# Performance work log

Measured on AMD Instinct MI355X. Metric: run time of the kernel, lower is better.

## Reference

```python
import jax, jax.numpy as jnp
import numpy as np

N_HEADS = 16

def setup_inputs() -> dict:
    key = jax.random.key(0)
    ks = jax.random.split(key, 4)
    B, T, C = 4, 2048, 1024
    x = jax.random.normal(ks[0], (B, T, C), dtype=jnp.float32)
    w_qkv = jax.random.normal(ks[1], (C, 3 * C), dtype=jnp.float32) * (1.0 / np.sqrt(C))
    b_qkv = jnp.zeros((3 * C,), dtype=jnp.float32)
    w_proj = jax.random.normal(ks[2], (C, C), dtype=jnp.float32) * (1.0 / np.sqrt(C))
    b_proj = jnp.zeros((C,), dtype=jnp.float32)
    return {"x": x, "w_qkv": w_qkv, "b_qkv": b_qkv, "w_proj": w_proj, "b_proj": b_proj}

def reference(x, w_qkv, b_qkv, w_proj, b_proj):
    B, T, C = x.shape
    H = N_HEADS
    d = C // H
    qkv = x @ w_qkv + b_qkv                       # [B,T,3C]
    q, k, v = jnp.split(qkv, 3, axis=-1)
    # [B,T,C] -> [B,H,T,d]
    q = q.reshape(B, T, H, d).transpose(0, 2, 1, 3)
    k = k.reshape(B, T, H, d).transpose(0, 2, 1, 3)
    v = v.reshape(B, T, H, d).transpose(0, 2, 1, 3)
    scale = 1.0 / np.sqrt(d).astype(np.float32)
    logits = jnp.einsum('bhqd,bhkd->bhqk', q, k) * scale  # [B,H,T,T]
    causal = jnp.tril(jnp.ones((T, T), dtype=bool))
    logits = jnp.where(causal, logits, jnp.finfo(logits.dtype).min)
    attn = jax.nn.softmax(logits, axis=-1)
    out = jnp.einsum('bhqk,bhkd->bhqd', attn, v)          # [B,H,T,d]
    out = out.transpose(0, 2, 1, 3).reshape(B, T, C)
    return out @ w_proj + b_proj
```

## Files before the change

### kernel.cpp

```cpp
#include <hip/hip_runtime.h>
#include <hip/hip_bf16.h>


typedef unsigned short u16;
typedef __bf16 bf16_t;
typedef bf16_t bf16x8 __attribute__((ext_vector_type(8)));
typedef float f32x4 __attribute__((ext_vector_type(4)));
typedef u16 u16x8 __attribute__((ext_vector_type(8)));
typedef const __attribute__((address_space(1))) void* as1cv;
typedef __attribute__((address_space(3))) void* as3v;

#define BB 4
#define TT 2048
#define CC 1024
#define HH 16
#define DD 64

static __device__ __forceinline__ u16 f2bf(float f) {
  union { float f; unsigned int u; } x; x.f = f;
  unsigned int u = x.u;
  u += 0x7fff + ((u >> 16) & 1);
  return (u16)(u >> 16);
}

static __device__ __forceinline__ unsigned int pack2(float lo, float hi) {
  return __builtin_amdgcn_perm(__float_as_uint(hi), __float_as_uint(lo),
                               0x07060302u);
}

__global__ __launch_bounds__(256) void prep(
    const float* __restrict__ x, u16* __restrict__ xb,
    const float* __restrict__ w_qkv, u16* __restrict__ wqkvT,
    const float* __restrict__ w_proj, u16* __restrict__ wprojT) {
  __shared__ float tile[32][33];
  const int id = blockIdx.x;
  if (id < 8192) {
    int i = (id * 256 + threadIdx.x) * 4;
    float4 v = *(const float4*)(x + i);
    ushort4 o;
    o.x = f2bf(v.x); o.y = f2bf(v.y); o.z = f2bf(v.z); o.w = f2bf(v.w);
    *(ushort4*)(xb + i) = o;
    return;
  }
  const float* in; u16* out; int N, n0, k0;
  if (id < 11264) {
    int i = id - 8192;
    in = w_qkv; out = wqkvT; N = 3072;
    n0 = (i % 96) * 32; k0 = (i / 96) * 32;
  } else {
    int i = id - 11264;
    in = w_proj; out = wprojT; N = 1024;
    n0 = (i & 31) * 32; k0 = (i >> 5) * 32;
  }
  const int tx = threadIdx.x & 31, ty = threadIdx.x >> 5;
#pragma unroll
  for (int i = 0; i < 32; i += 8)
    tile[ty + i][tx] = in[(size_t)(k0 + ty + i) * N + n0 + tx];
  __syncthreads();
#pragma unroll
  for (int i = 0; i < 32; i += 8)
    out[(size_t)(n0 + ty + i) * 1024 + k0 + tx] = f2bf(tile[tx][ty + i]);
}

__global__ __launch_bounds__(256) void gemm_bt(
    const u16* __restrict__ A, const u16* __restrict__ Bt,
    const float* __restrict__ bias,
    int M, int N, int K, int mode,
    u16* __restrict__ qb, u16* __restrict__ kb, u16* __restrict__ vt,
    float* __restrict__ outf) {
  __shared__ u16 As[128][64];
  __shared__ u16 Bs[128][64];
  const int tid = threadIdx.x;
  const int lane = tid & 63, wave = tid >> 6;
  const int quad = lane >> 4, l16 = lane & 15;
  const int wy = wave >> 1, wx = wave & 1;
  const int mpc = (M >> 7) >> 3;
  const int id = blockIdx.x;
  const int xcd = id & 7, w = id >> 3;
  const int mi = xcd * mpc + (w % mpc);
  const int ni = w / mpc;
  const int m0 = mi * 128, n0 = ni * 128;
  const int srow = lane >> 3, sblk = (lane & 7) ^ (lane >> 3);
  const int rsw = l16 & 7;

  f32x4 acc[4][4] = {};

  for (int k0 = 0; k0 < K; k0 += 64) {
#pragma unroll
    for (int i = 0; i < 4; i++) {
      int lr = wave * 32 + i * 8;
      int row = lr + srow;
      __builtin_amdgcn_global_load_lds(
          (as1cv)(A + (size_t)(m0 + row) * K + k0 + sblk * 8),
          (as3v)(&As[lr][0]), 16, 0, 0);
      __builtin_amdgcn_global_load_lds(
          (as1cv)(Bt + (size_t)(n0 + row) * K + k0 + sblk * 8),
          (as3v)(&Bs[lr][0]), 16, 0, 0);
    }
    __syncthreads();
#pragma unroll
    for (int ks = 0; ks < 2; ks++) {
      const int pcol = ((ks * 4 + quad) ^ rsw) * 8;
      bf16x8 af[4], bfr[4];
#pragma unroll
      for (int i = 0; i < 4; i++)
        af[i] = *(const bf16x8*)&As[wy * 64 + i * 16 + l16][pcol];
#pragma unroll
      for (int j = 0; j < 4; j++)
        bfr[j] = *(const bf16x8*)&Bs[wx * 64 + j * 16 + l16][pcol];
#pragma unroll
      for (int i = 0; i < 4; i++)
#pragma unroll
        for (int j = 0; j < 4; j++)
          acc[i][j] = __builtin_amdgcn_mfma_f32_16x16x32_bf16(af[i], bfr[j], acc[i][j], 0, 0, 0);
    }
    __syncthreads();
  }

  if (mode == 1) {
#pragma unroll
    for (int i = 0; i < 4; i++)
#pragma unroll
      for (int j = 0; j < 4; j++) {
        int nn = n0 + wx * 64 + j * 16 + l16;
        float bv = bias[nn];
#pragma unroll
        for (int r = 0; r < 4; r++) {
          int mm = m0 + wy * 64 + i * 16 + quad * 4 + r;
          outf[(size_t)mm * N + nn] = acc[i][j][r] + bv;
        }
      }
  } else {
    const int b = m0 >> 11;
    const int tb = (m0 & 2047) + wy * 64 + quad * 4;
    if (n0 < 1024) {
#pragma unroll
      for (int j = 0; j < 4; j++) {
        int nn = n0 + wx * 64 + j * 16 + l16;
        int h = nn >> 6, dd = nn & 63;
        float bv = bias[nn];
        u16* base = qb + ((size_t)(b * HH + h) * TT) * DD + dd;
#pragma unroll
        for (int i = 0; i < 4; i++)
#pragma unroll
          for (int r = 0; r < 4; r++)
            base[(size_t)(tb + i * 16 + r) * DD] =
                f2bf((acc[i][j][r] + bv) * 0.1803368801111f);
      }
    } else if (n0 < 2048) {
#pragma unroll
      for (int j = 0; j < 4; j++) {
        int nn = n0 + wx * 64 + j * 16 + l16;
        int rem = nn & 1023, h = rem >> 6, dd = rem & 63;
        float bv = bias[nn];
        u16* base = kb + ((size_t)(b * HH + h) * TT) * DD + dd;
#pragma unroll
        for (int i = 0; i < 4; i++)
#pragma unroll
          for (int r = 0; r < 4; r++)
            base[(size_t)(tb + i * 16 + r) * DD] = f2bf(acc[i][j][r] + bv);
      }
    } else {
#pragma unroll
      for (int j = 0; j < 4; j++) {
        int nn = n0 + wx * 64 + j * 16 + l16;
        int rem = nn & 1023, h = rem >> 6, dd = rem & 63;
        float bv = bias[nn];
        u16* base = vt + ((size_t)(b * HH + h) * DD + dd) * TT;
#pragma unroll
        for (int i = 0; i < 4; i++)
#pragma unroll
          for (int r = 0; r < 4; r++)
            base[tb + i * 16 + r] = f2bf(acc[i][j][r] + bv);
      }
    }
  }
}

__global__ __launch_bounds__(256) void gemm_proj64(
    const u16* __restrict__ A, const u16* __restrict__ Bt,
    const float* __restrict__ bias, float* __restrict__ outf) {
  constexpr int N = 1024, K = 1024;
  __shared__ u16 As[64][64];
  __shared__ u16 Bs[128][64];
  const int tid = threadIdx.x;
  const int lane = tid & 63, wave = tid >> 6;
  const int quad = lane >> 4, l16 = lane & 15;
  const int wy = wave >> 1, wx = wave & 1;
  const int id = blockIdx.x;
  const int xcd = id & 7, w = id >> 3;
  const int m0 = (xcd * 16 + (w & 15)) * 64, n0 = (w >> 4) * 128;
  const int srow = lane >> 3, sblk = (lane & 7) ^ (lane >> 3);
  const int rsw = l16 & 7;

  f32x4 acc[2][4] = {};

  for (int k0 = 0; k0 < K; k0 += 64) {
#pragma unroll
    for (int i = 0; i < 2; i++) {
      int lr = wave * 16 + i * 8;
      __builtin_amdgcn_global_load_lds(
          (as1cv)(A + (size_t)(m0 + lr + srow) * K + k0 + sblk * 8),
          (as3v)(&As[lr][0]), 16, 0, 0);
    }
#pragma unroll
    for (int i = 0; i < 4; i++) {
      int lr = wave * 32 + i * 8;
      __builtin_amdgcn_global_load_lds(
          (as1cv)(Bt + (size_t)(n0 + lr + srow) * K + k0 + sblk * 8),
          (as3v)(&Bs[lr][0]), 16, 0, 0);
    }
    __syncthreads();
#pragma unroll
    for (int ks = 0; ks < 2; ks++) {
      const int pcol = ((ks * 4 + quad) ^ rsw) * 8;
      bf16x8 af[2], bfr[4];
#pragma unroll
      for (int i = 0; i < 2; i++)
        af[i] = *(const bf16x8*)&As[wy * 32 + i * 16 + l16][pcol];
#pragma unroll
      for (int j = 0; j < 4; j++)
        bfr[j] = *(const bf16x8*)&Bs[wx * 64 + j * 16 + l16][pcol];
#pragma unroll
      for (int i = 0; i < 2; i++)
#pragma unroll
        for (int j = 0; j < 4; j++)
          acc[i][j] = __builtin_amdgcn_mfma_f32_16x16x32_bf16(af[i], bfr[j], acc[i][j], 0, 0, 0);
    }
    __syncthreads();
  }

#pragma unroll
  for (int i = 0; i < 2; i++)
#pragma unroll
    for (int j = 0; j < 4; j++) {
      int nn = n0 + wx * 64 + j * 16 + l16;
      float bv = bias[nn];
#pragma unroll
      for (int r = 0; r < 4; r++) {
        int mm = m0 + wy * 32 + i * 16 + quad * 4 + r;
        outf[(size_t)mm * N + nn] = acc[i][j][r] + bv;
      }
    }
}

__global__ __launch_bounds__(256, 3) void attn_kernel(
    const u16* __restrict__ q_buf, const u16* __restrict__ k_buf,
    const u16* __restrict__ v_t, u16* __restrict__ attn_out) {
  __shared__ __align__(16) u16 Ks[2][64][64];
  __shared__ __align__(16) u16 Vs[2][64][64];
  __shared__ __align__(16) u16 Pl[4][2][16][64];
  const int tid = threadIdx.x;
  const int lane = tid & 63, wave = tid >> 6;
  const int quad = lane >> 4, l16 = lane & 15;
  const int bh = blockIdx.x;
  const int b = bh >> 4, h = bh & 15;
  const int perm16[16] = {15,14,13,12, 0,1,2,3, 11,10,9,8, 4,5,6,7};
  const int tile = perm16[blockIdx.y];
  const int qt0 = tile * 128;
  const int qw = qt0 + wave * 32;
  const u16* Q = q_buf + (size_t)bh * TT * DD;
  const u16* Kp = k_buf + (size_t)bh * TT * DD;
  const u16* Vt = v_t + (size_t)bh * DD * TT;

  const int srow = lane >> 3;
  const int sblk = (lane & 7) ^ srow;
  const int swz = l16 & 7;

  bf16x8 qf[2][2];
#pragma unroll
  for (int f = 0; f < 2; f++)
#pragma unroll
    for (int h2 = 0; h2 < 2; h2++)
      qf[f][h2] = *(const bf16x8*)(Q + (size_t)(qw + f * 16 + l16) * DD + h2 * 32 + quad * 8);

  f32x4 o[2][4] = {};
  float l_p[2] = {0.f, 0.f};

  const int my_end = qw + 32;
  const int kv_stop = qt0 + 128;
  for (int kv0 = 0; kv0 < kv_stop; kv0 += 128) {
#pragma unroll
    for (int hh = 0; hh < 2; hh++)
#pragma unroll
      for (int i = 0; i < 2; i++) {
        int r = wave * 16 + i * 8 + srow;
        __builtin_amdgcn_global_load_lds(
            (as1cv)(Kp + (size_t)(kv0 + hh * 64 + r) * DD + sblk * 8),
            (as3v)(&Ks[hh][wave * 16 + i * 8][0]), 16, 0, 0);
        __builtin_amdgcn_global_load_lds(
            (as1cv)(Vt + (size_t)r * TT + kv0 + hh * 64 + sblk * 8),
            (as3v)(&Vs[hh][wave * 16 + i * 8][0]), 16, 0, 0);
      }
    __syncthreads();

#pragma unroll
    for (int hh = 0; hh < 2; hh++) {
      const int kb0 = kv0 + hh * 64;
      if (kb0 < my_end) {
        const bool edge = (kb0 + 63 > qw);
        f32x4 s[2][4] = {};
        __builtin_amdgcn_s_setprio(1);
#pragma unroll
        for (int kg = 0; kg < 4; kg++) {
          bf16x8 ka = *(const bf16x8*)&Ks[hh][kg * 16 + l16][(quad ^ swz) * 8];
          bf16x8 kb2 = *(const bf16x8*)&Ks[hh][kg * 16 + l16][((4 + quad) ^ swz) * 8];
#pragma unroll
          for (int f = 0; f < 2; f++) {
            s[f][kg] = __builtin_amdgcn_mfma_f32_16x16x32_bf16(ka, qf[f][0], s[f][kg], 0, 0, 0);
            s[f][kg] = __builtin_amdgcn_mfma_f32_16x16x32_bf16(kb2, qf[f][1], s[f][kg], 0, 0, 0);
          }
        }
        __builtin_amdgcn_s_setprio(0);
#pragma unroll
        for (int f = 0; f < 2; f++) {
          const int qi = qw + f * 16 + l16;
#pragma unroll
          for (int kg = 0; kg < 4; kg++) {
            float v0 = s[f][kg][0], v1 = s[f][kg][1], v2 = s[f][kg][2], v3 = s[f][kg][3];
            if (edge) {
              int kvb = kb0 + kg * 16 + quad * 4;
              v0 = (kvb + 0 <= qi) ? v0 : -1e30f;
              v1 = (kvb + 1 <= qi) ? v1 : -1e30f;
              v2 = (kvb + 2 <= qi) ? v2 : -1e30f;
              v3 = (kvb + 3 <= qi) ? v3 : -1e30f;
            }
            float e0 = __builtin_amdgcn_exp2f(v0);
            float e1 = __builtin_amdgcn_exp2f(v1);
            float e2 = __builtin_amdgcn_exp2f(v2);
            float e3 = __builtin_amdgcn_exp2f(v3);
            l_p[f] += (e0 + e1) + (e2 + e3);
            uint2 pk;
            pk.x = pack2(e0, e1);
            pk.y = pack2(e2, e3);
            *(uint2*)&Pl[wave][f][l16][((kg * 2 + (quad >> 1)) ^ swz) * 8 + (quad & 1) * 4] = pk;
          }
        }
        __threadfence_block();
#pragma unroll
        for (int c = 0; c < 2; c++) {
          bf16x8 pa0 = *(const bf16x8*)&Pl[wave][0][l16][((c * 4 + quad) ^ swz) * 8];
          bf16x8 pa1 = *(const bf16x8*)&Pl[wave][1][l16][((c * 4 + quad) ^ swz) * 8];
          __builtin_amdgcn_s_setprio(1);
#pragma unroll
          for (int g = 0; g < 4; g++) {
            bf16x8 vr = *(const bf16x8*)&Vs[hh][g * 16 + l16][((c * 4 + quad) ^ swz) * 8];
            o[0][g] = __builtin_amdgcn_mfma_f32_16x16x32_bf16(vr, pa0, o[0][g], 0, 0, 0);
            o[1][g] = __builtin_amdgcn_mfma_f32_16x16x32_bf16(vr, pa1, o[1][g], 0, 0, 0);
          }
          __builtin_amdgcn_s_setprio(0);
        }
      }
    }
    __syncthreads();
  }

#pragma unroll
  for (int f = 0; f < 2; f++) {
    float l = l_p[f];
    l += __shfl_xor(l, 16);
    l += __shfl_xor(l, 32);
    float inv_l = 1.0f / l;
    int trow = qw + f * 16 + l16;
#pragma unroll
    for (int g = 0; g < 4; g++) {
      ushort4 st;
      st.x = f2bf(o[f][g][0] * inv_l);
      st.y = f2bf(o[f][g][1] * inv_l);
      st.z = f2bf(o[f][g][2] * inv_l);
      st.w = f2bf(o[f][g][3] * inv_l);
      *(ushort4*)(attn_out + ((size_t)(b * TT + trow)) * CC + h * DD + g * 16 + quad * 4) = st;
    }
  }
}

extern "C" void kernel_launch(void* const* d_in, const int* in_sizes, int n_in,
                              void* d_out, int out_size, void* d_ws, size_t ws_size,
                              hipStream_t stream) {
  const float* x = (const float*)d_in[0];
  const float* w_qkv = (const float*)d_in[1];
  const float* b_qkv = (const float*)d_in[2];
  const float* w_proj = (const float*)d_in[3];
  const float* b_proj = (const float*)d_in[4];
  float* out = (float*)d_out;
  char* ws = (char*)d_ws;

  u16* wqkvT = (u16*)(ws);
  u16* wprojT = (u16*)(ws + 6291456);
  u16* qb = (u16*)(ws + 8388608);
  u16* kb = (u16*)(ws + 25165824);
  u16* vt = (u16*)(ws + 41943040);
  u16* ao = (u16*)(ws + 58720256);
  u16* xb = ao;

  prep<<<dim3(12288), 256, 0, stream>>>(x, xb, w_qkv, wqkvT, w_proj, wprojT);
  gemm_bt<<<dim3(1536), 256, 0, stream>>>(xb, wqkvT, b_qkv, 8192, 3072, 1024, 0,
                                          qb, kb, vt, nullptr);
  attn_kernel<<<dim3(64, 16), 256, 0, stream>>>(qb, kb, vt, ao);
  gemm_proj64<<<dim3(1024), 256, 0, stream>>>(ao, wprojT, b_proj, out);
}
```

Before: 247.9 us.

## Replace QKV GEMM with 256x256 double-buffered ping-pong pipelined kernel

Replaces the 128x128 single-buffered QKV projection GEMM with a 256x256-tile, 512-thread kernel. It double-buffers LDS and interleaves async global-to-LDS loads with MFMA phases, using barriers, s_setprio and partial vmcnt waits. V-transpose stores are also vectorised to ushort4. The goal is to hide memory latency and raise data reuse per tile. The cost is a large LDS footprint (128KB per block), fewer blocks (384), and fragile hand-tuned synchronisation.

Result: faster. 238.6 us (-3.8%).

```diff
diff --git a/kernel.cpp b/kernel.cpp
--- a/kernel.cpp
+++ b/kernel.cpp
@@ -62,116 +62,230 @@
     out[(size_t)(n0 + ty + i) * 1024 + k0 + tx] = f2bf(tile[tx][ty + i]);
 }
 
-__global__ __launch_bounds__(256) void gemm_bt(
+__global__ __launch_bounds__(512, 2) void gemm_qkv256(
     const u16* __restrict__ A, const u16* __restrict__ Bt,
     const float* __restrict__ bias,
-    int M, int N, int K, int mode,
-    u16* __restrict__ qb, u16* __restrict__ kb, u16* __restrict__ vt,
-    float* __restrict__ outf) {
-  __shared__ u16 As[128][64];
-  __shared__ u16 Bs[128][64];
+    u16* __restrict__ qb, u16* __restrict__ kb, u16* __restrict__ vt) {
+  constexpr int K = 1024;
+  __shared__ u16 As[2][256][64];
+  __shared__ u16 Bs[2][256][64];
   const int tid = threadIdx.x;
   const int lane = tid & 63, wave = tid >> 6;
   const int quad = lane >> 4, l16 = lane & 15;
-  const int wy = wave >> 1, wx = wave & 1;
-  const int mpc = (M >> 7) >> 3;
+  const int wr = wave >> 2, wc = wave & 3;
+  const int rsw = l16 & 7;
+  const int srow8 = tid >> 3;
+  const int sblk = (lane & 7) ^ (lane >> 3);
+
   const int id = blockIdx.x;
-  const int xcd = id & 7, w = id >> 3;
-  const int mi = xcd * mpc + (w % mpc);
-  const int ni = w / mpc;
-  const int m0 = mi * 128, n0 = ni * 128;
-  const int srow = lane >> 3, sblk = (lane & 7) ^ (lane >> 3);
-  const int rsw = l16 & 7;
-
-  f32x4 acc[4][4] = {};
-
-  for (int k0 = 0; k0 < K; k0 += 64) {
-#pragma unroll
-    for (int i = 0; i < 4; i++) {
-      int lr = wave * 32 + i * 8;
-      int row = lr + srow;
-      __builtin_amdgcn_global_load_lds(
-          (as1cv)(A + (size_t)(m0 + row) * K + k0 + sblk * 8),
-          (as3v)(&As[lr][0]), 16, 0, 0);
-      __builtin_amdgcn_global_load_lds(
-          (as1cv)(Bt + (size_t)(n0 + row) * K + k0 + sblk * 8),
-          (as3v)(&Bs[lr][0]), 16, 0, 0);
-    }
-    __syncthreads();
-#pragma unroll
-    for (int ks = 0; ks < 2; ks++) {
-      const int pcol = ((ks * 4 + quad) ^ rsw) * 8;
-      bf16x8 af[4], bfr[4];
-#pragma unroll
-      for (int i = 0; i < 4; i++)
-        af[i] = *(const bf16x8*)&As[wy * 64 + i * 16 + l16][pcol];
-#pragma unroll
-      for (int j = 0; j < 4; j++)
-        bfr[j] = *(const bf16x8*)&Bs[wx * 64 + j * 16 + l16][pcol];
-#pragma unroll
-      for (int i = 0; i < 4; i++)
-#pragma unroll
-        for (int j = 0; j < 4; j++)
-          acc[i][j] = __builtin_amdgcn_mfma_f32_16x16x32_bf16(af[i], bfr[j], acc[i][j], 0, 0, 0);
-    }
-    __syncthreads();
-  }
-
-  if (mode == 1) {
-#pragma unroll
-    for (int i = 0; i < 4; i++)
-#pragma unroll
-      for (int j = 0; j < 4; j++) {
-        int nn = n0 + wx * 64 + j * 16 + l16;
-        float bv = bias[nn];
-#pragma unroll
-        for (int r = 0; r < 4; r++) {
-          int mm = m0 + wy * 64 + i * 16 + quad * 4 + r;
-          outf[(size_t)mm * N + nn] = acc[i][j][r] + bv;
-        }
-      }
+  const int ch = id & 7, w = id >> 3;
+  const int mi = (ch & 3) * 8 + w / 6;
+  const int ni = (ch >> 2) * 6 + w % 6;
+  const int m0 = mi * 256, n0 = ni * 256;
+
+  const u16* Ab = A + (size_t)(m0 + srow8) * K + sblk * 8;
+  const u16* Bb = Bt + (size_t)(n0 + srow8) * K + sblk * 8;
+
+#define STA(bufd, line, kt) __builtin_amdgcn_global_load_lds(              \
+    (as1cv)(Ab + ((line) * 64) * K + (kt) * 64),                           \
+    (as3v)(&As[bufd][(line) * 64 + wave * 8][0]), 16, 0, 0)
+#define STB(bufd, line, kt) __builtin_amdgcn_global_load_lds(              \
+    (as1cv)(Bb + ((line) * 64) * K + (kt) * 64),                           \
+    (as3v)(&Bs[bufd][(line) * 64 + wave * 8][0]), 16, 0, 0)
+#define LDA(bufd, mf, ks) (*(const bf16x8*)&As[bufd][wr * 128 + (mf) * 16 + l16] \
+                                              [(((ks) * 4 + quad) ^ rsw) * 8])
+#define LDB(bufd, nf, ks) (*(const bf16x8*)&Bs[bufd][wc * 64 + (nf) * 16 + l16]  \
+                                              [(((ks) * 4 + quad) ^ rsw) * 8])
+#define MFMA(af, bf, c) __builtin_amdgcn_mfma_f32_16x16x32_bf16(af, bf, c, 0, 0, 0)
+
+  STA(0, 0, 0); STA(0, 1, 0); STA(0, 2, 0); STA(0, 3, 0);
+  STB(0, 0, 0); STB(0, 1, 0); STB(0, 2, 0); STB(0, 3, 0);
+  STB(1, 0, 1); STB(1, 1, 1); STB(1, 2, 1); STB(1, 3, 1);
+  asm volatile("s_waitcnt vmcnt(4)" ::: "memory");
+  __builtin_amdgcn_s_barrier();
+
+  f32x4 acc[8][4] = {};
+  bf16x8 a[4][2], b0[2][2], b1[2][2];
+
+#pragma unroll 1
+  for (int i = 0; i < 8; ++i) {
+    const int t1 = 2 * i + 1, t2 = 2 * i + 2, t3 = 2 * i + 3;
+    const bool more = (i < 7);
+
+#pragma unroll
+    for (int mf = 0; mf < 4; mf++) { a[mf][0] = LDA(0, mf, 0); a[mf][1] = LDA(0, mf, 1); }
+#pragma unroll
+    for (int nf = 0; nf < 2; nf++) { b0[nf][0] = LDB(0, nf, 0); b0[nf][1] = LDB(0, nf, 1); }
+    STA(1, 0, t1); STA(1, 1, t1);
+    __builtin_amdgcn_s_barrier();
+    __builtin_amdgcn_s_setprio(1);
+#pragma unroll
+    for (int mf = 0; mf < 4; mf++)
+#pragma unroll
+      for (int nf = 0; nf < 2; nf++) {
+        acc[mf][nf] = MFMA(a[mf][0], b0[nf][0], acc[mf][nf]);
+        acc[mf][nf] = MFMA(a[mf][1], b0[nf][1], acc[mf][nf]);
+      }
+    __builtin_amdgcn_s_setprio(0);
+    __builtin_amdgcn_s_barrier();
+
+#pragma unroll
+    for (int nf = 0; nf < 2; nf++) { b1[nf][0] = LDB(0, 2 + nf, 0); b1[nf][1] = LDB(0, 2 + nf, 1); }
+    STA(1, 2, t1); STA(1, 3, t1);
+    __builtin_amdgcn_s_barrier();
+    __builtin_amdgcn_s_setprio(1);
+#pragma unroll
+    for (int mf = 0; mf < 4; mf++)
+#pragma unroll
+      for (int nf = 0; nf < 2; nf++) {
+        acc[mf][2 + nf] = MFMA(a[mf][0], b1[nf][0], acc[mf][2 + nf]);
+        acc[mf][2 + nf] = MFMA(a[mf][1], b1[nf][1], acc[mf][2 + nf]);
+      }
+    __builtin_amdgcn_s_setprio(0);
+    __builtin_amdgcn_s_barrier();
+
+#pragma unroll
+    for (int mf = 0; mf < 4; mf++) { a[mf][0] = LDA(0, 4 + mf, 0); a[mf][1] = LDA(0, 4 + mf, 1); }
+    if (more) { STB(0, 0, t2); STB(0, 1, t2); }
+    __builtin_amdgcn_s_barrier();
+    __builtin_amdgcn_s_setprio(1);
+#pragma unroll
+    for (int mf = 0; mf < 4; mf++)
+#pragma unroll
+      for (int nf = 0; nf < 2; nf++) {
+        acc[4 + mf][2 + nf] = MFMA(a[mf][0], b1[nf][0], acc[4 + mf][2 + nf]);
+        acc[4 + mf][2 + nf] = MFMA(a[mf][1], b1[nf][1], acc[4 + mf][2 + nf]);
+      }
+    __builtin_amdgcn_s_setprio(0);
+    __builtin_amdgcn_s_barrier();
+
+    if (more) { STB(0, 2, t2); STB(0, 3, t2); }
+    __builtin_amdgcn_s_barrier();
+    __builtin_amdgcn_s_setprio(1);
+#pragma unroll
+    for (int mf = 0; mf < 4; mf++)
+#pragma unroll
+      for (int nf = 0; nf < 2; nf++) {
+        acc[4 + mf][nf] = MFMA(a[mf][0], b0[nf][0], acc[4 + mf][nf]);
+        acc[4 + mf][nf] = MFMA(a[mf][1], b0[nf][1], acc[4 + mf][nf]);
+      }
+    __builtin_amdgcn_s_setprio(0);
+    if (more) asm volatile("s_waitcnt vmcnt(4)" ::: "memory");
+    else      asm volatile("s_waitcnt vmcnt(0)" ::: "memory");
+    __builtin_amdgcn_s_barrier();
+
+#pragma unroll
+    for (int mf = 0; mf < 4; mf++) { a[mf][0] = LDA(1, mf, 0); a[mf][1] = LDA(1, mf, 1); }
+#pragma unroll
+    for (int nf = 0; nf < 2; nf++) { b0[nf][0] = LDB(1, nf, 0); b0[nf][1] = LDB(1, nf, 1); }
+    if (more) { STA(0, 0, t2); STA(0, 1, t2); }
+    __builtin_amdgcn_s_barrier();
+    __builtin_amdgcn_s_setprio(1);
+#pragma unroll
+    for (int mf = 0; mf < 4; mf++)
+#pragma unroll
+      for (int nf = 0; nf < 2; nf++) {
+        acc[mf][nf] = MFMA(a[mf][0], b0[nf][0], acc[mf][nf]);
+        acc[mf][nf] = MFMA(a[mf][1], b0[nf][1], acc[mf][nf]);
+      }
+    __builtin_amdgcn_s_setprio(0);
+    __builtin_amdgcn_s_barrier();
+
+#pragma unroll
+    for (int nf = 0; nf < 2; nf++) { b1[nf][0] = LDB(1, 2 + nf, 0); b1[nf][1] = LDB(1, 2 + nf, 1); }
+    if (more) { STA(0, 2, t2); STA(0, 3, t2); }
+    __builtin_amdgcn_s_barrier();
+    __builtin_amdgcn_s_setprio(1);
+#pragma unroll
+    for (int mf = 0; mf < 4; mf++)
+#pragma unroll
+      for (int nf = 0; nf < 2; nf++) {
+        acc[mf][2 + nf] = MFMA(a[mf][0], b1[nf][0], acc[mf][2 + nf]);
+        acc[mf][2 + nf] = MFMA(a[mf][1], b1[nf][1], acc[mf][2 + nf]);
+      }
+    __builtin_amdgcn_s_setprio(0);
+    __builtin_amdgcn_s_barrier();
+
+#pragma unroll
+    for (int mf = 0; mf < 4; mf++) { a[mf][0] = LDA(1, 4 + mf, 0); a[mf][1] = LDA(1, 4 + mf, 1); }
+    if (more) { STB(1, 0, t3); STB(1, 1, t3); }
+    __builtin_amdgcn_s_barrier();
+    __builtin_amdgcn_s_setprio(1);
+#pragma unroll
+    for (int mf = 0; mf < 4; mf++)
+#pragma unroll
+      for (int nf = 0; nf < 2; nf++) {
+        acc[4 + mf][2 + nf] = MFMA(a[mf][0], b1[nf][0], acc[4 + mf][2 + nf]);
+        acc[4 + mf][2 + nf] = MFMA(a[mf][1], b1[nf][1], acc[4 + mf][2 + nf]);
+      }
+    __builtin_amdgcn_s_setprio(0);
+    __builtin_amdgcn_s_barrier();
+
+    if (more) { STB(1, 2, t3); STB(1, 3, t3); }
+    __builtin_amdgcn_s_barrier();
+    __builtin_amdgcn_s_setprio(1);
+#pragma unroll
+    for (int mf = 0; mf < 4; mf++)
+#pragma unroll
+      for (int nf = 0; nf < 2; nf++) {
+        acc[4 + mf][nf] = MFMA(a[mf][0], b0[nf][0], acc[4 + mf][nf]);
+        acc[4 + mf][nf] = MFMA(a[mf][1], b0[nf][1], acc[4 + mf][nf]);
+      }
+    __builtin_amdgcn_s_setprio(0);
+    if (more) asm volatile("s_waitcnt vmcnt(4)" ::: "memory");
+    __builtin_amdgcn_s_barrier();
+  }
+#undef STA
+#undef STB
+#undef LDA
+#undef LDB
+#undef MFMA
+
+  const int b = m0 >> 11;
+  const int tb = (m0 & 2047) + wr * 128 + quad * 4;
+  const int seg = n0 >> 10;
+  if (seg == 0) {
+#pragma unroll
+    for (int nf = 0; nf < 4; nf++) {
+      int nn = n0 + wc * 64 + nf * 16 + l16;
+      int hh = (nn & 1023) >> 6, dd = nn & 63;
+      float bv = bias[nn];
+      u16* base = qb + ((size_t)(b * HH + hh) * TT) * DD + dd;
+#pragma unroll
+      for (int mf = 0; mf < 8; mf++)
+#pragma unroll
+        for (int r = 0; r < 4; r++)
+          base[(size_t)(tb + mf * 16 + r) * DD] =
+              f2bf((acc[mf][nf][r] + bv) * 0.1803368801111f);
+    }
+  } else if (seg == 1) {
+#pragma unroll
+    for (int nf = 0; nf < 4; nf++) {
+      int nn = n0 + wc * 64 + nf * 16 + l16;
+      int hh = (nn & 1023) >> 6, dd = nn & 63;
+      float bv = bias[nn];
+      u16* base = kb + ((size_t)(b * HH + hh) * TT) * DD + dd;
+#pragma unroll
+      for (int mf = 0; mf < 8; mf++)
+#pragma unroll
+        for (int r = 0; r < 4; r++)
+          base[(size_t)(tb + mf * 16 + r) * DD] = f2bf(acc[mf][nf][r] + bv);
+    }
   } else {
-    const int b = m0 >> 11;
-    const int tb = (m0 & 2047) + wy * 64 + quad * 4;
-    if (n0 < 1024) {
-#pragma unroll
-      for (int j = 0; j < 4; j++) {
-        int nn = n0 + wx * 64 + j * 16 + l16;
-        int h = nn >> 6, dd = nn & 63;
-        float bv = bias[nn];
-        u16* base = qb + ((size_t)(b * HH + h) * TT) * DD + dd;
-#pragma unroll
-        for (int i = 0; i < 4; i++)
-#pragma unroll
-          for (int r = 0; r < 4; r++)
-            base[(size_t)(tb + i * 16 + r) * DD] =
-                f2bf((acc[i][j][r] + bv) * 0.1803368801111f);
-      }
-    } else if (n0 < 2048) {
-#pragma unroll
-      for (int j = 0; j < 4; j++) {
-        int nn = n0 + wx * 64 + j * 16 + l16;
-        int rem = nn & 1023, h = rem >> 6, dd = rem & 63;
-        float bv = bias[nn];
-        u16* base = kb + ((size_t)(b * HH + h) * TT) * DD + dd;
-#pragma unroll
-        for (int i = 0; i < 4; i++)
-#pragma unroll
-          for (int r = 0; r < 4; r++)
-            base[(size_t)(tb + i * 16 + r) * DD] = f2bf(acc[i][j][r] + bv);
-      }
-    } else {
-#pragma unroll
-      for (int j = 0; j < 4; j++) {
-        int nn = n0 + wx * 64 + j * 16 + l16;
-        int rem = nn & 1023, h = rem >> 6, dd = rem & 63;
-        float bv = bias[nn];
-        u16* base = vt + ((size_t)(b * HH + h) * DD + dd) * TT;
-#pragma unroll
-        for (int i = 0; i < 4; i++)
-#pragma unroll
-          for (int r = 0; r < 4; r++)
-            base[tb + i * 16 + r] = f2bf(acc[i][j][r] + bv);
+#pragma unroll
+    for (int nf = 0; nf < 4; nf++) {
+      int nn = n0 + wc * 64 + nf * 16 + l16;
+      int hh = (nn & 1023) >> 6, dd = nn & 63;
+      float bv = bias[nn];
+      u16* base = vt + ((size_t)(b * HH + hh) * DD + dd) * TT + tb;
+#pragma unroll
+      for (int mf = 0; mf < 8; mf++) {
+        ushort4 st;
+        st.x = f2bf(acc[mf][nf][0] + bv);
+        st.y = f2bf(acc[mf][nf][1] + bv);
+        st.z = f2bf(acc[mf][nf][2] + bv);
+        st.w = f2bf(acc[mf][nf][3] + bv);
+        *(ushort4*)(base + mf * 16) = st;
       }
     }
   }
@@ -394,8 +508,7 @@
   u16* xb = ao;
 
   prep<<<dim3(12288), 256, 0, stream>>>(x, xb, w_qkv, wqkvT, w_proj, wprojT);
-  gemm_bt<<<dim3(1536), 256, 0, stream>>>(xb, wqkvT, b_qkv, 8192, 3072, 1024, 0,
-                                          qb, kb, vt, nullptr);
+  gemm_qkv256<<<dim3(384), 512, 0, stream>>>(xb, wqkvT, b_qkv, qb, kb, vt);
   attn_kernel<<<dim3(64, 16), 256, 0, stream>>>(qb, kb, vt, ao);
   gemm_proj64<<<dim3(1024), 256, 0, stream>>>(ao, wprojT, b_proj, out);
 }
```
